# Kernel tuning notes

Hardware: AMD Instinct MI355X
Metric: run time of the kernel (lower is better)

Reference implementation:

```python
import jax, jax.numpy as jnp
import numpy as np

N_NODES = 100000
N_EDGES = 1250000
D_FEAT = 64


def setup_inputs() -> dict:
    key = jax.random.key(0)
    k1, k2, k3 = jax.random.split(key, 3)
    inputs = jax.random.normal(k1, (N_NODES, D_FEAT), dtype=jnp.float32)
    src = jax.random.randint(k2, (N_EDGES,), 0, N_NODES, dtype=jnp.int32)
    dst = jax.random.randint(k3, (N_EDGES,), 0, N_NODES, dtype=jnp.int32)
    return {"inputs": inputs, "src": src, "dst": dst}


def reference(inputs, src, dst):
    # copy_src: message on each edge is the source node's feature -> gather
    msgs = inputs[src]  # [E, d]
    # gcn_reduce: max over mailbox (incoming messages) per destination node
    agg = jax.ops.segment_max(msgs, dst, num_segments=N_NODES)  # [N, d], -inf for empty
    # Nodes receiving no messages keep their original feature (DGL recv semantics)
    indeg = jax.ops.segment_sum(jnp.ones((src.shape[0],), dtype=jnp.int32), dst,
                                num_segments=N_NODES)  # [N]
    v_feature = jnp.where((indeg > 0)[:, None], agg, inputs)  # [N, d]
    return jnp.concatenate([inputs, v_feature], axis=1)  # [N, 2d]
```

## Files before the change

### kernel.cpp

```cpp
#include <hip/hip_runtime.h>
#include <math.h>

#define D_FEAT 64
#define SCAN_BLOCK 1024
#define NG 8
#define NR 8


__device__ __forceinline__ int block_scan_excl_1024(int v, int* smem16) {
    int lane = threadIdx.x & 63;
    int wid  = threadIdx.x >> 6;
    int x = v;
    #pragma unroll
    for (int d = 1; d < 64; d <<= 1) {
        int t = __shfl_up(x, d, 64);
        if (lane >= d) x += t;
    }
    if (lane == 63) smem16[wid] = x;
    __syncthreads();
    if (wid == 0) {
        int s = (lane < 16) ? smem16[lane] : 0;
        #pragma unroll
        for (int d = 1; d < 16; d <<= 1) {
            int t = __shfl_up(s, d, 64);
            if (lane >= d) s += t;
        }
        if (lane < 16) smem16[lane] = s;
    }
    __syncthreads();
    int base = (wid > 0) ? smem16[wid - 1] : 0;
    return base + x - v;
}


__global__ void count_group_kernel(const int* __restrict__ dst,
                                   int* __restrict__ priv,
                                   int n_nodes, int n_edges, int egroup) {
    int g = blockIdx.x & (NG - 1);
    int c = blockIdx.x >> 3;
    int nchunks = gridDim.x >> 3;
    int ebeg = g * egroup;
    int eend = ebeg + egroup; if (eend > n_edges) eend = n_edges;
    int* cnt = priv + (size_t)g * n_nodes;
    int stride = nchunks * blockDim.x;
    for (int e = ebeg + c * blockDim.x + threadIdx.x; e < eend; e += stride) {
        atomicAdd(&cnt[dst[e]], 1);
    }
}

__global__ void hist_part_kernel(const int* __restrict__ dst,
                                 int* __restrict__ counts,
                                 int n_edges, int nodes_per_range) {
    int r = blockIdx.x & (NR - 1);
    int c = blockIdx.x / NR;
    int nchunks = gridDim.x / NR;
    int lo = r * nodes_per_range;
    int hi = lo + nodes_per_range;
    int stride = nchunks * blockDim.x;
    for (int e = c * blockDim.x + threadIdx.x; e < n_edges; e += stride) {
        int d = dst[e];
        if (d >= lo && d < hi) atomicAdd(&counts[d], 1);
    }
}


__global__ void scanA_fused_kernel(int* __restrict__ priv,
                                   int* __restrict__ offsets,
                                   int* __restrict__ blocksums, int n_nodes) {
    __shared__ int smem16[16];
    int i = blockIdx.x * SCAN_BLOCK + threadIdx.x;
    int total = 0;
    if (i < n_nodes) {
        int run = 0;
        #pragma unroll
        for (int g = 0; g < NG; ++g) {
            size_t idx = (size_t)g * n_nodes + i;
            int t = priv[idx];
            priv[idx] = run;
            run += t;
        }
        total = run;
    }
    int excl = block_scan_excl_1024(total, smem16);
    if (i < n_nodes) offsets[i] = excl;
    if (threadIdx.x == SCAN_BLOCK - 1) blocksums[blockIdx.x] = excl + total;
}

__global__ void scanA_plain_kernel(const int* __restrict__ counts,
                                   int* __restrict__ offsets,
                                   int* __restrict__ blocksums, int n) {
    __shared__ int smem16[16];
    int i = blockIdx.x * SCAN_BLOCK + threadIdx.x;
    int v = (i < n) ? counts[i] : 0;
    int e = block_scan_excl_1024(v, smem16);
    if (i < n) offsets[i] = e;
    if (threadIdx.x == SCAN_BLOCK - 1) blocksums[blockIdx.x] = e + v;
}

__global__ void scanB_kernel(int* __restrict__ blocksums, int nb) {
    __shared__ int smem16[16];
    int v = ((int)threadIdx.x < nb) ? blocksums[threadIdx.x] : 0;
    int e = block_scan_excl_1024(v, smem16);
    if ((int)threadIdx.x < nb) blocksums[threadIdx.x] = e;
}

__global__ void scanC_kernel(int* __restrict__ offsets,
                             const int* __restrict__ blocksums,
                             int n, int n_edges) {
    int i = blockIdx.x * SCAN_BLOCK + threadIdx.x;
    if (i < n) offsets[i] += blocksums[blockIdx.x];
    if (i == 0) offsets[n] = n_edges;
}

__global__ void scanC_plain_kernel(int* __restrict__ offsets,
                                   int* __restrict__ cursor,
                                   const int* __restrict__ blocksums,
                                   int n, int n_edges) {
    int i = blockIdx.x * SCAN_BLOCK + threadIdx.x;
    if (i < n) {
        int o = offsets[i] + blocksums[blockIdx.x];
        offsets[i] = o;
        cursor[i] = o;
    }
    if (i == 0) offsets[n] = n_edges;
}


__global__ void scatter_rg_kernel(const int* __restrict__ src,
                                  const int* __restrict__ dst,
                                  const int* __restrict__ offsets,
                                  int* __restrict__ priv,
                                  int* __restrict__ sorted_src,
                                  int n_nodes, int n_edges, int egroup,
                                  int nodes_per_range) {
    int r = blockIdx.x & (NR - 1);
    int g = (blockIdx.x >> 3) & (NG - 1);
    int c = blockIdx.x >> 6;
    int nchunks = gridDim.x >> 6;
    int lo = r * nodes_per_range;
    int hi = lo + nodes_per_range;
    int ebeg = g * egroup;
    int eend = ebeg + egroup; if (eend > n_edges) eend = n_edges;
    int* cur = priv + (size_t)g * n_nodes;
    int stride = nchunks * blockDim.x;
    for (int e = ebeg + c * blockDim.x + threadIdx.x; e < eend; e += stride) {
        int d = dst[e];
        if (d >= lo && d < hi) {
            int pos = offsets[d] + atomicAdd(&cur[d], 1);
            sorted_src[pos] = src[e];
        }
    }
}

__global__ void scatter_part_kernel(const int* __restrict__ src,
                                    const int* __restrict__ dst,
                                    int* __restrict__ cursor,
                                    int* __restrict__ sorted_src,
                                    int n_edges, int nodes_per_range) {
    int r = blockIdx.x & (NR - 1);
    int c = blockIdx.x / NR;
    int nchunks = gridDim.x / NR;
    int lo = r * nodes_per_range;
    int hi = lo + nodes_per_range;
    int stride = nchunks * blockDim.x;
    for (int e = c * blockDim.x + threadIdx.x; e < n_edges; e += stride) {
        int d = dst[e];
        if (d >= lo && d < hi) {
            int pos = atomicAdd(&cursor[d], 1);
            sorted_src[pos] = src[e];
        }
    }
}


__global__ void pull_max_kernel(const float* __restrict__ inp,
                                const int* __restrict__ offsets,
                                const int* __restrict__ sorted_src,
                                float* __restrict__ out, int n_nodes) {
    int gtid = blockIdx.x * blockDim.x + threadIdx.x;
    int node = gtid >> 6;
    if (node >= n_nodes) return;
    int lane = threadIdx.x & 63;
    int g = lane >> 4;
    int l = lane & 15;

    int beg = offsets[node];
    int end = offsets[node + 1];

    const float4* inp4 = reinterpret_cast<const float4*>(inp);
    float4 own = inp4[(size_t)node * 16 + l];

    float4 m;
    m.x = -INFINITY; m.y = -INFINITY; m.z = -INFINITY; m.w = -INFINITY;
    int j = beg + g;
    for (; j + 4 < end; j += 8) {
        int s0 = sorted_src[j];
        int s1 = sorted_src[j + 4];
        float4 v0 = inp4[(size_t)s0 * 16 + l];
        float4 v1 = inp4[(size_t)s1 * 16 + l];
        m.x = fmaxf(m.x, fmaxf(v0.x, v1.x));
        m.y = fmaxf(m.y, fmaxf(v0.y, v1.y));
        m.z = fmaxf(m.z, fmaxf(v0.z, v1.z));
        m.w = fmaxf(m.w, fmaxf(v0.w, v1.w));
    }
    if (j < end) {
        int s = sorted_src[j];
        float4 v = inp4[(size_t)s * 16 + l];
        m.x = fmaxf(m.x, v.x);
        m.y = fmaxf(m.y, v.y);
        m.z = fmaxf(m.z, v.z);
        m.w = fmaxf(m.w, v.w);
    }
    m.x = fmaxf(m.x, __shfl_xor(m.x, 16, 64));
    m.y = fmaxf(m.y, __shfl_xor(m.y, 16, 64));
    m.z = fmaxf(m.z, __shfl_xor(m.z, 16, 64));
    m.w = fmaxf(m.w, __shfl_xor(m.w, 16, 64));
    m.x = fmaxf(m.x, __shfl_xor(m.x, 32, 64));
    m.y = fmaxf(m.y, __shfl_xor(m.y, 32, 64));
    m.z = fmaxf(m.z, __shfl_xor(m.z, 32, 64));
    m.w = fmaxf(m.w, __shfl_xor(m.w, 32, 64));

    if (beg == end) m = own;

    float4* out4 = reinterpret_cast<float4*>(out);
    if (lane < 16) {
        out4[(size_t)node * 32 + l] = own;
    } else if (lane < 32) {
        out4[(size_t)node * 32 + 16 + l] = m;
    }
}


extern "C" void kernel_launch(void* const* d_in, const int* in_sizes, int n_in,
                              void* d_out, int out_size, void* d_ws, size_t ws_size,
                              hipStream_t stream) {
    const float* inp = (const float*)d_in[0];
    const int* src = (const int*)d_in[1];
    const int* dst = (const int*)d_in[2];
    float* out = (float*)d_out;

    int n_nodes = in_sizes[0] / D_FEAT;
    int n_edges = in_sizes[1];

    int nScanBlocks = (n_nodes + SCAN_BLOCK - 1) / SCAN_BLOCK;
    int nodes_per_range = (n_nodes + NR - 1) / NR;
    int egroup = (n_edges + NG - 1) / NG;

    int* ws = (int*)d_ws;
    size_t need_main = ((size_t)NG * n_nodes + (size_t)(n_nodes + 1) +
                        (size_t)nScanBlocks + (size_t)n_edges) * sizeof(int);

    if (ws_size >= need_main) {
        int* priv = ws;
        int* offsets = ws + (size_t)NG * n_nodes;
        int* blocksums = offsets + n_nodes + 1;
        int* sorted_src = blocksums + nScanBlocks;

        hipMemsetAsync(priv, 0, (size_t)NG * n_nodes * sizeof(int), stream);
        count_group_kernel<<<NG * 256, 256, 0, stream>>>(dst, priv, n_nodes,
                                                         n_edges, egroup);
        scanA_fused_kernel<<<nScanBlocks, SCAN_BLOCK, 0, stream>>>(priv, offsets,
                                                                   blocksums, n_nodes);
        scanB_kernel<<<1, SCAN_BLOCK, 0, stream>>>(blocksums, nScanBlocks);
        scanC_kernel<<<nScanBlocks, SCAN_BLOCK, 0, stream>>>(offsets, blocksums,
                                                             n_nodes, n_edges);
        scatter_rg_kernel<<<NR * NG * 32, 256, 0, stream>>>(src, dst, offsets,
                                                            priv, sorted_src,
                                                            n_nodes, n_edges,
                                                            egroup, nodes_per_range);
        {
            int total = n_nodes * 64;
            pull_max_kernel<<<(total + 255) / 256, 256, 0, stream>>>(
                inp, offsets, sorted_src, out, n_nodes);
        }
    } else {
        int* counts = ws;
        int* offsets = ws + n_nodes;
        int* blocksums = offsets + n_nodes + 1;
        int* sorted_src = blocksums + nScanBlocks;

        hipMemsetAsync(counts, 0, (size_t)n_nodes * sizeof(int), stream);
        hist_part_kernel<<<NR * 256, 256, 0, stream>>>(dst, counts, n_edges,
                                                       nodes_per_range);
        scanA_plain_kernel<<<nScanBlocks, SCAN_BLOCK, 0, stream>>>(counts, offsets,
                                                                   blocksums, n_nodes);
        scanB_kernel<<<1, SCAN_BLOCK, 0, stream>>>(blocksums, nScanBlocks);
        scanC_plain_kernel<<<nScanBlocks, SCAN_BLOCK, 0, stream>>>(offsets, counts,
                                                                   blocksums,
                                                                   n_nodes, n_edges);
        scatter_part_kernel<<<NR * 256, 256, 0, stream>>>(src, dst, counts,
                                                          sorted_src, n_edges,
                                                          nodes_per_range);
        {
            int total = n_nodes * 64;
            pull_max_kernel<<<(total + 255) / 256, 256, 0, stream>>>(
                inp, offsets, sorted_src, out, n_nodes);
        }
    }
}
```

Baseline: 245.6 us.

## Fuse CSR build stages into one cooperative kernel with grid syncs

Replaces the memset, count, three scan kernels and scatter with a single cooperative kernel that uses grid.sync between phases, launched with up to 512 blocks of 1024 threads. The aim is to remove several kernel launch gaps and tail bubbles on the small-scan stages. The trade-offs are lower parallelism per phase, a serialized single-block scanB, the cost of grid-wide barriers, and a fixed 1024-entry blocksums layout. The low-workspace fallback path is dropped, and the original multi-kernel sequence remains as the fallback if the cooperative launch fails.

```diff
diff --git a/kernel.cpp b/kernel.cpp
--- a/kernel.cpp
+++ b/kernel.cpp
@@ -1,5 +1,8 @@
 #include <hip/hip_runtime.h>
+#include <hip/hip_cooperative_groups.h>
 #include <math.h>
+
+namespace cg = cooperative_groups;
 
 #define D_FEAT 64
 #define SCAN_BLOCK 1024
@@ -30,6 +33,95 @@
     __syncthreads();
     int base = (wid > 0) ? smem16[wid - 1] : 0;
     return base + x - v;
+}
+
+
+__global__ __launch_bounds__(1024, 8)
+void build_csr_coop(const int* __restrict__ src, const int* __restrict__ dst,
+                    int* __restrict__ priv, int* __restrict__ offsets,
+                    int* __restrict__ blocksums, int* __restrict__ sorted_src,
+                    int n_nodes, int n_edges, int egroup, int nodes_per_range,
+                    int ntiles) {
+    cg::grid_group grid = cg::this_grid();
+    __shared__ int smem16[16];
+    const int tid = threadIdx.x;
+    const int bid = blockIdx.x;
+    const int nb  = gridDim.x;
+
+    {
+        int total = NG * n_nodes;
+        for (int i = bid * SCAN_BLOCK + tid; i < total; i += nb * SCAN_BLOCK)
+            priv[i] = 0;
+    }
+    grid.sync();
+
+    {
+        int g = bid & (NG - 1);
+        int c = bid >> 3;
+        int nchunks = nb >> 3;
+        int ebeg = g * egroup;
+        int eend = ebeg + egroup; if (eend > n_edges) eend = n_edges;
+        int* cnt = priv + (size_t)g * n_nodes;
+        int stride = nchunks * SCAN_BLOCK;
+        for (int e = ebeg + c * SCAN_BLOCK + tid; e < eend; e += stride)
+            atomicAdd(&cnt[dst[e]], 1);
+    }
+    grid.sync();
+
+    for (int tile = bid; tile < ntiles; tile += nb) {
+        int i = tile * SCAN_BLOCK + tid;
+        int total = 0;
+        if (i < n_nodes) {
+            int run = 0;
+            #pragma unroll
+            for (int g = 0; g < NG; ++g) {
+                size_t idx = (size_t)g * n_nodes + i;
+                int t = priv[idx];
+                priv[idx] = run;
+                run += t;
+            }
+            total = run;
+        }
+        int excl = block_scan_excl_1024(total, smem16);
+        if (i < n_nodes) offsets[i] = excl;
+        if (tid == SCAN_BLOCK - 1) blocksums[tile] = excl + total;
+        __syncthreads();
+    }
+    grid.sync();
+
+    if (bid == 0) {
+        int v = (tid < ntiles) ? blocksums[tid] : 0;
+        int e = block_scan_excl_1024(v, smem16);
+        if (tid < ntiles) blocksums[tid] = e;
+    }
+    grid.sync();
+
+    for (int tile = bid; tile < ntiles; tile += nb) {
+        int i = tile * SCAN_BLOCK + tid;
+        if (i < n_nodes) offsets[i] += blocksums[tile];
+    }
+    if (bid == 0 && tid == 0) offsets[n_nodes] = n_edges;
+    grid.sync();
+
+    {
+        int r = bid & (NR - 1);
+        int g = (bid >> 3) & (NG - 1);
+        int c = bid >> 6;
+        int nchunks = nb >> 6;
+        int lo = r * nodes_per_range;
+        int hi = lo + nodes_per_range;
+        int ebeg = g * egroup;
+        int eend = ebeg + egroup; if (eend > n_edges) eend = n_edges;
+        int* cur = priv + (size_t)g * n_nodes;
+        int stride = nchunks * SCAN_BLOCK;
+        for (int e = ebeg + c * SCAN_BLOCK + tid; e < eend; e += stride) {
+            int d = dst[e];
+            if (d >= lo && d < hi) {
+                int pos = offsets[d] + atomicAdd(&cur[d], 1);
+                sorted_src[pos] = src[e];
+            }
+        }
+    }
 }
 
 
@@ -47,22 +139,6 @@
         atomicAdd(&cnt[dst[e]], 1);
     }
 }
-
-__global__ void hist_part_kernel(const int* __restrict__ dst,
-                                 int* __restrict__ counts,
-                                 int n_edges, int nodes_per_range) {
-    int r = blockIdx.x & (NR - 1);
-    int c = blockIdx.x / NR;
-    int nchunks = gridDim.x / NR;
-    int lo = r * nodes_per_range;
-    int hi = lo + nodes_per_range;
-    int stride = nchunks * blockDim.x;
-    for (int e = c * blockDim.x + threadIdx.x; e < n_edges; e += stride) {
-        int d = dst[e];
-        if (d >= lo && d < hi) atomicAdd(&counts[d], 1);
-    }
-}
-
 
 __global__ void scanA_fused_kernel(int* __restrict__ priv,
                                    int* __restrict__ offsets,
@@ -86,17 +162,6 @@
     if (threadIdx.x == SCAN_BLOCK - 1) blocksums[blockIdx.x] = excl + total;
 }
 
-__global__ void scanA_plain_kernel(const int* __restrict__ counts,
-                                   int* __restrict__ offsets,
-                                   int* __restrict__ blocksums, int n) {
-    __shared__ int smem16[16];
-    int i = blockIdx.x * SCAN_BLOCK + threadIdx.x;
-    int v = (i < n) ? counts[i] : 0;
-    int e = block_scan_excl_1024(v, smem16);
-    if (i < n) offsets[i] = e;
-    if (threadIdx.x == SCAN_BLOCK - 1) blocksums[blockIdx.x] = e + v;
-}
-
 __global__ void scanB_kernel(int* __restrict__ blocksums, int nb) {
     __shared__ int smem16[16];
     int v = ((int)threadIdx.x < nb) ? blocksums[threadIdx.x] : 0;
@@ -111,20 +176,6 @@
     if (i < n) offsets[i] += blocksums[blockIdx.x];
     if (i == 0) offsets[n] = n_edges;
 }
-
-__global__ void scanC_plain_kernel(int* __restrict__ offsets,
-                                   int* __restrict__ cursor,
-                                   const int* __restrict__ blocksums,
-                                   int n, int n_edges) {
-    int i = blockIdx.x * SCAN_BLOCK + threadIdx.x;
-    if (i < n) {
-        int o = offsets[i] + blocksums[blockIdx.x];
-        offsets[i] = o;
-        cursor[i] = o;
-    }
-    if (i == 0) offsets[n] = n_edges;
-}
-
 
 __global__ void scatter_rg_kernel(const int* __restrict__ src,
                                   const int* __restrict__ dst,
@@ -152,26 +203,6 @@
     }
 }
 
-__global__ void scatter_part_kernel(const int* __restrict__ src,
-                                    const int* __restrict__ dst,
-                                    int* __restrict__ cursor,
-                                    int* __restrict__ sorted_src,
-                                    int n_edges, int nodes_per_range) {
-    int r = blockIdx.x & (NR - 1);
-    int c = blockIdx.x / NR;
-    int nchunks = gridDim.x / NR;
-    int lo = r * nodes_per_range;
-    int hi = lo + nodes_per_range;
-    int stride = nchunks * blockDim.x;
-    for (int e = c * blockDim.x + threadIdx.x; e < n_edges; e += stride) {
-        int d = dst[e];
-        if (d >= lo && d < hi) {
-            int pos = atomicAdd(&cursor[d], 1);
-            sorted_src[pos] = src[e];
-        }
-    }
-}
-
 
 __global__ void pull_max_kernel(const float* __restrict__ inp,
                                 const int* __restrict__ offsets,
@@ -242,59 +273,61 @@
     int n_nodes = in_sizes[0] / D_FEAT;
     int n_edges = in_sizes[1];
 
-    int nScanBlocks = (n_nodes + SCAN_BLOCK - 1) / SCAN_BLOCK;
+    int ntiles = (n_nodes + SCAN_BLOCK - 1) / SCAN_BLOCK;
     int nodes_per_range = (n_nodes + NR - 1) / NR;
     int egroup = (n_edges + NG - 1) / NG;
 
     int* ws = (int*)d_ws;
-    size_t need_main = ((size_t)NG * n_nodes + (size_t)(n_nodes + 1) +
-                        (size_t)nScanBlocks + (size_t)n_edges) * sizeof(int);
-
-    if (ws_size >= need_main) {
-        int* priv = ws;
-        int* offsets = ws + (size_t)NG * n_nodes;
-        int* blocksums = offsets + n_nodes + 1;
-        int* sorted_src = blocksums + nScanBlocks;
-
+    int* priv = ws;
+    int* offsets = ws + (size_t)NG * n_nodes;
+    int* blocksums = offsets + n_nodes + 1;
+    int* sorted_src = blocksums + 1024;
+
+    bool coop_done = false;
+    if (ntiles <= 1024) {
+        int maxB = 0;
+        hipError_t qerr = hipOccupancyMaxActiveBlocksPerMultiprocessor(
+            &maxB, build_csr_coop, SCAN_BLOCK, 0);
+        if (qerr == hipSuccess && maxB > 0) {
+            int nb = maxB * 256;
+            if (nb > 512) nb = 512;
+            nb &= ~63;
+            if (nb >= 64) {
+                const int* a_src = src; const int* a_dst = dst;
+                int* a_priv = priv; int* a_off = offsets;
+                int* a_bs = blocksums; int* a_ss = sorted_src;
+                int a_n = n_nodes, a_e = n_edges, a_eg = egroup;
+                int a_npr = nodes_per_range, a_nt = ntiles;
+                void* args[] = {(void*)&a_src, (void*)&a_dst, (void*)&a_priv,
+                                (void*)&a_off, (void*)&a_bs, (void*)&a_ss,
+                                (void*)&a_n, (void*)&a_e, (void*)&a_eg,
+                                (void*)&a_npr, (void*)&a_nt};
+                hipError_t lerr = hipLaunchCooperativeKernel(
+                    (const void*)build_csr_coop, dim3(nb), dim3(SCAN_BLOCK),
+                    args, 0, stream);
+                coop_done = (lerr == hipSuccess);
+            }
+        }
+    }
+
+    if (!coop_done) {
         hipMemsetAsync(priv, 0, (size_t)NG * n_nodes * sizeof(int), stream);
         count_group_kernel<<<NG * 256, 256, 0, stream>>>(dst, priv, n_nodes,
                                                          n_edges, egroup);
-        scanA_fused_kernel<<<nScanBlocks, SCAN_BLOCK, 0, stream>>>(priv, offsets,
-                                                                   blocksums, n_nodes);
-        scanB_kernel<<<1, SCAN_BLOCK, 0, stream>>>(blocksums, nScanBlocks);
-        scanC_kernel<<<nScanBlocks, SCAN_BLOCK, 0, stream>>>(offsets, blocksums,
-                                                             n_nodes, n_edges);
+        scanA_fused_kernel<<<ntiles, SCAN_BLOCK, 0, stream>>>(priv, offsets,
+                                                              blocksums, n_nodes);
+        scanB_kernel<<<1, SCAN_BLOCK, 0, stream>>>(blocksums, ntiles);
+        scanC_kernel<<<ntiles, SCAN_BLOCK, 0, stream>>>(offsets, blocksums,
+                                                        n_nodes, n_edges);
         scatter_rg_kernel<<<NR * NG * 32, 256, 0, stream>>>(src, dst, offsets,
                                                             priv, sorted_src,
                                                             n_nodes, n_edges,
                                                             egroup, nodes_per_range);
-        {
-            int total = n_nodes * 64;
-            pull_max_kernel<<<(total + 255) / 256, 256, 0, stream>>>(
-                inp, offsets, sorted_src, out, n_nodes);
-        }
-    } else {
-        int* counts = ws;
-        int* offsets = ws + n_nodes;
-        int* blocksums = offsets + n_nodes + 1;
-        int* sorted_src = blocksums + nScanBlocks;
-
-        hipMemsetAsync(counts, 0, (size_t)n_nodes * sizeof(int), stream);
-        hist_part_kernel<<<NR * 256, 256, 0, stream>>>(dst, counts, n_edges,
-                                                       nodes_per_range);
-        scanA_plain_kernel<<<nScanBlocks, SCAN_BLOCK, 0, stream>>>(counts, offsets,
-                                                                   blocksums, n_nodes);
-        scanB_kernel<<<1, SCAN_BLOCK, 0, stream>>>(blocksums, nScanBlocks);
-        scanC_plain_kernel<<<nScanBlocks, SCAN_BLOCK, 0, stream>>>(offsets, counts,
-                                                                   blocksums,
-                                                                   n_nodes, n_edges);
-        scatter_part_kernel<<<NR * 256, 256, 0, stream>>>(src, dst, counts,
-                                                          sorted_src, n_edges,
-                                                          nodes_per_range);
-        {
-            int total = n_nodes * 64;
-            pull_max_kernel<<<(total + 255) / 256, 256, 0, stream>>>(
-                inp, offsets, sorted_src, out, n_nodes);
-        }
-    }
-}
+    }
+
+    {
+        int total = n_nodes * 64;
+        pull_max_kernel<<<(total + 255) / 256, 256, 0, stream>>>(
+            inp, offsets, sorted_src, out, n_nodes);
+    }
+}
```

Measured after the change: 499.1 us. 2.03x slower.
